# Optimization experiments

Hardware: AMD Instinct MI355X
Metric: run time of the kernel (lower is better)

## Reference

```python
import jax, jax.numpy as jnp
import numpy as np

B, T, H, V, L = 256, 64, 1024, 128, 32  # batch, enc len, hidden, vocab, max decode len


def setup_inputs() -> dict:
    key = jax.random.key(0)
    ks = jax.random.split(key, 12)
    s = 1.0 / np.sqrt(H)
    inp = {
        "inputs": jax.random.randint(ks[0], (B, T), 0, V, dtype=jnp.int32),
        "max_len": L,
        # encoder params
        "enc_emb": jax.random.normal(ks[1], (V, H), jnp.float32) * 0.02,
        "enc_W": jax.random.normal(ks[2], (H, 4 * H), jnp.float32) * s,
        "enc_U": jax.random.normal(ks[3], (H, 4 * H), jnp.float32) * s,
        "enc_b": jnp.zeros((4 * H,), jnp.float32),
        # decoder params
        "dec_emb": jax.random.normal(ks[4], (V, H), jnp.float32) * 0.02,
        "dec_W": jax.random.normal(ks[5], (H, 4 * H), jnp.float32) * s,
        "dec_U": jax.random.normal(ks[6], (H, 4 * H), jnp.float32) * s,
        "dec_b": jnp.zeros((4 * H,), jnp.float32),
        # output projection
        "out_W": jax.random.normal(ks[7], (H, V), jnp.float32) * s,
        "out_b": jnp.zeros((V,), jnp.float32),
    }
    return inp


def _lstm_step(h, c, x, W, U, b):
    # Keras gate order: input, forget, cell, output
    z = x @ W + h @ U + b  # [B, 4H]
    i, f, g, o = jnp.split(z, 4, axis=-1)
    i = jax.nn.sigmoid(i)
    f = jax.nn.sigmoid(f)
    g = jnp.tanh(g)
    o = jax.nn.sigmoid(o)
    c2 = f * c + i * g
    h2 = o * jnp.tanh(c2)
    return h2, c2


def reference(inputs, max_len, enc_emb, enc_W, enc_U, enc_b,
              dec_emb, dec_W, dec_U, dec_b, out_W, out_b):
    batch = inputs.shape[0]
    hid = enc_W.shape[0]
    vocab = dec_emb.shape[0]
    delimiter = vocab - 1

    # ---- Encoder (mask_zero=True: masked steps carry state through) ----
    x_emb = enc_emb[inputs]                     # [B, T, H]
    mask = (inputs != 0)                        # [B, T]

    def enc_scan(carry, xs):
        h, c = carry
        x_t, m_t = xs                           # [B,H], [B]
        h2, c2 = _lstm_step(h, c, x_t, enc_W, enc_U, enc_b)
        m = m_t[:, None]
        return (jnp.where(m, h2, h), jnp.where(m, c2, c)), None

    h0 = jnp.zeros((batch, hid), x_emb.dtype)
    c0 = jnp.zeros((batch, hid), x_emb.dtype)
    (h, c), _ = jax.lax.scan(enc_scan, (h0, c0),
                             (x_emb.transpose(1, 0, 2), mask.T))

    # ---- Greedy decoder: embed -> LSTM -> dense -> softmax -> argmax ----
    def dec_scan(carry, _):
        h, c, tok = carry
        x = dec_emb[tok]                        # [B, H]
        m = (tok != 0)[:, None]
        h2, c2 = _lstm_step(h, c, x, dec_W, dec_U, dec_b)
        h2 = jnp.where(m, h2, h)
        c2 = jnp.where(m, c2, c)
        y = jax.nn.softmax(h2 @ out_W + out_b)  # [B, V]
        tok2 = jnp.argmax(y, axis=-1).astype(jnp.int32)
        return (h2, c2, tok2), (y, tok2)

    tok0 = jnp.full((batch,), delimiter, jnp.int32)
    _, (ys, toks) = jax.lax.scan(dec_scan, (h, c, tok0), None, length=max_len)
    outputs = ys.transpose(1, 0, 2)             # [B, max_len, V]
    return outputs, toks
```

## Files before the change

### kernel.cpp

```cpp
#include <hip/hip_runtime.h>
#include <hip/hip_bf16.h>

namespace {
constexpr int BATCH = 256;
constexpr int TENC  = 64;
constexpr int HID   = 1024;
constexpr int VOC   = 128;
constexpr int LDEC  = 32;
constexpr int G4    = 4 * HID;
}

using short8 = __attribute__((ext_vector_type(8))) short;
using f32x4  = __attribute__((ext_vector_type(4))) float;

__device__ __forceinline__ void async16(const void* g, void* l) {
  __builtin_amdgcn_global_load_lds(
      (const __attribute__((address_space(1))) void*)g,
      (__attribute__((address_space(3))) void*)l, 16, 0, 0);
}

__device__ __forceinline__ unsigned short f2bf(float x) {
  unsigned int u = __float_as_uint(x);
  return (unsigned short)((u + 0x7fffu + ((u >> 16) & 1u)) >> 16);
}
__device__ __forceinline__ float bf2f(unsigned short h) {
  return __uint_as_float(((unsigned int)h) << 16);
}

__global__ __launch_bounds__(256) void k_init(float* __restrict__ h0,
                                              float* __restrict__ c,
                                              unsigned int* __restrict__ hpk0,
                                              int* __restrict__ tok) {
  int i = blockIdx.x * 256 + threadIdx.x;
  h0[i] = 0.f;
  c[i]  = 0.f;
  hpk0[i] = 0u;
  if (i < BATCH) tok[i] = VOC - 1;
}

__global__ __launch_bounds__(256) void k_split_u(
    const float* __restrict__ enc_U, const float* __restrict__ dec_U,
    unsigned short* __restrict__ enc_hi, unsigned short* __restrict__ enc_lo,
    unsigned short* __restrict__ dec_hi, unsigned short* __restrict__ dec_lo) {
  const float* U;
  unsigned short *hi_p, *lo_p;
  if (blockIdx.y == 0) { U = enc_U; hi_p = enc_hi; lo_p = enc_lo; }
  else                 { U = dec_U; hi_p = dec_hi; lo_p = dec_lo; }
  const int gid = blockIdx.x * 256 + threadIdx.x;
  const int lanep = gid & 63;
  const int kq = lanep >> 4, coln = lanep & 15;
  const int u = gid >> 6;
  const int f = u & 7;
  const int v2 = u >> 3;
  const int ks = v2 & 31, ct = v2 >> 5;
  const int n = (f >> 1) * HID + ct * 32 + (f & 1) * 16 + coln;
  const int kbase = ks * 32 + kq * 8;

  unsigned short hv[8], lv[8];
#pragma unroll
  for (int kk = 0; kk < 8; ++kk) {
    const float x = U[(size_t)(kbase + kk) * G4 + n];
    hv[kk] = f2bf(x);
    lv[kk] = f2bf(x - bf2f(hv[kk]));
  }
  *(short8*)(hi_p + (size_t)gid * 8) = *(short8*)hv;
  *(short8*)(lo_p + (size_t)gid * 8) = *(short8*)lv;
}

__global__ __launch_bounds__(256) void k_precompute(
    const float* __restrict__ enc_emb, const float* __restrict__ enc_W,
    const float* __restrict__ enc_b,   const float* __restrict__ dec_emb,
    const float* __restrict__ dec_W,   const float* __restrict__ dec_b,
    float* __restrict__ P_enc, float* __restrict__ P_dec) {
  const float* emb; const float* W; const float* bias; float* P;
  if (blockIdx.z == 0) { emb = enc_emb; W = enc_W; bias = enc_b; P = P_enc; }
  else                 { emb = dec_emb; W = dec_W; bias = dec_b; P = P_dec; }

  __shared__ float A_s[2][64][32];
  __shared__ float B_s[2][32][64];

  const int t    = threadIdx.x;
  const int col0 = blockIdx.x * 64;
  const int v0   = blockIdx.y * 64;
  const int tx   = t & 15;
  const int ty   = t >> 4;
  const int a_row = t >> 3, a_kq = (t & 7) * 4;
  const int b_k   = t >> 4, b_cq = (t & 15) * 4;

  float acc[4][4];
#pragma unroll
  for (int r = 0; r < 4; ++r)
#pragma unroll
    for (int j = 0; j < 4; ++j) acc[r][j] = 0.f;

  async16(&emb[(v0 + a_row) * HID + a_kq], &A_s[0][a_row][a_kq]);
  async16(&emb[(v0 + 32 + a_row) * HID + a_kq], &A_s[0][32 + a_row][a_kq]);
  async16(&W[b_k * G4 + col0 + b_cq], &B_s[0][b_k][b_cq]);
  async16(&W[(16 + b_k) * G4 + col0 + b_cq], &B_s[0][16 + b_k][b_cq]);

  for (int tile = 0; tile < 32; ++tile) {
    const int buf = tile & 1;
    __syncthreads();
    if (tile < 31) {
      const int nb = buf ^ 1;
      const int k0 = (tile + 1) * 32;
      async16(&emb[(v0 + a_row) * HID + k0 + a_kq], &A_s[nb][a_row][a_kq]);
      async16(&emb[(v0 + 32 + a_row) * HID + k0 + a_kq],
              &A_s[nb][32 + a_row][a_kq]);
      async16(&W[(k0 + b_k) * G4 + col0 + b_cq], &B_s[nb][b_k][b_cq]);
      async16(&W[(k0 + 16 + b_k) * G4 + col0 + b_cq],
              &B_s[nb][16 + b_k][b_cq]);
    }
#pragma unroll
    for (int k4 = 0; k4 < 32; k4 += 4) {
      float4 av[4];
#pragma unroll
      for (int r = 0; r < 4; ++r)
        av[r] = *(const float4*)&A_s[buf][ty * 4 + r][k4];
#pragma unroll
      for (int q = 0; q < 4; ++q) {
        const float4 b = *(const float4*)&B_s[buf][k4 + q][tx * 4];
#pragma unroll
        for (int r = 0; r < 4; ++r) {
          const float a = ((const float*)&av[r])[q];
          acc[r][0] += a * b.x;
          acc[r][1] += a * b.y;
          acc[r][2] += a * b.z;
          acc[r][3] += a * b.w;
        }
      }
    }
  }

  const float4 b4 = *(const float4*)&bias[col0 + tx * 4];
#pragma unroll
  for (int r = 0; r < 4; ++r) {
    float4 o;
    o.x = acc[r][0] + b4.x;
    o.y = acc[r][1] + b4.y;
    o.z = acc[r][2] + b4.z;
    o.w = acc[r][3] + b4.w;
    *(float4*)&P[(v0 + ty * 4 + r) * G4 + col0 + tx * 4] = o;
  }
}

__global__ __launch_bounds__(256, 1) void k_cell(
    const float* __restrict__ h_in, float* __restrict__ h_out,
    float* __restrict__ c,
    const unsigned short* __restrict__ Upk_hi,
    const unsigned short* __restrict__ Upk_lo,
    const unsigned short* __restrict__ hpk_in,
    unsigned short* __restrict__ hpk_out,
    const float* __restrict__ P, const int* __restrict__ tok_idx,
    int tok_stride) {
  const int bx = blockIdx.x;
  const int ct = bx & 31;
  const int rt = bx >> 5;
  const int j0 = ct * 32;
  const int r0 = rt * 32;
  const int t    = threadIdx.x;
  const int lane = t & 63;
  const int g    = t >> 6;

  __shared__ float z_s[32][132];

  const unsigned short* pa[2][2];
  const unsigned short* pb[2][2];
#pragma unroll
  for (int m = 0; m < 2; ++m)
#pragma unroll
    for (int s = 0; s < 2; ++s)
      pa[m][s] = hpk_in + ((((s * 32) * 16 + (rt * 2 + m)) * 64 + lane) << 3);
#pragma unroll
  for (int nf = 0; nf < 2; ++nf) {
    pb[nf][0] = Upk_hi + (((ct * 32 * 8 + (g * 2 + nf)) * 64 + lane) << 3);
    pb[nf][1] = Upk_lo + (((ct * 32 * 8 + (g * 2 + nf)) * 64 + lane) << 3);
  }
  constexpr int ASTR = 16 * 64 * 8;
  constexpr int BSTR = 8 * 64 * 8;

  short8 a[4][2][2], b[4][2][2];
  f32x4 acc[2][2];
#pragma unroll
  for (int m = 0; m < 2; ++m)
#pragma unroll
    for (int n = 0; n < 2; ++n) acc[m][n] = (f32x4){0.f, 0.f, 0.f, 0.f};

#define LOADT(T, p)                                                          \
  {                                                                          \
    _Pragma("unroll") for (int m = 0; m < 2; ++m)                            \
        _Pragma("unroll") for (int s = 0; s < 2; ++s)                        \
            a[p][m][s] = *(const short8*)(pa[m][s] + (T) * ASTR);            \
    _Pragma("unroll") for (int nf = 0; nf < 2; ++nf)                         \
        _Pragma("unroll") for (int s = 0; s < 2; ++s)                        \
            b[p][nf][s] = *(const short8*)(pb[nf][s] + (T) * BSTR);          \
  }
#define MFMAT(p)                                                             \
  _Pragma("unroll") for (int m = 0; m < 2; ++m)                              \
      _Pragma("unroll") for (int n = 0; n < 2; ++n) {                        \
    acc[m][n] = __builtin_amdgcn_mfma_f32_16x16x32_bf16(                     \
        a[p][m][0], b[p][n][0], acc[m][n], 0, 0, 0);                         \
    acc[m][n] = __builtin_amdgcn_mfma_f32_16x16x32_bf16(                     \
        a[p][m][0], b[p][n][1], acc[m][n], 0, 0, 0);                         \
    acc[m][n] = __builtin_amdgcn_mfma_f32_16x16x32_bf16(                     \
        a[p][m][1], b[p][n][0], acc[m][n], 0, 0, 0);                         \
    acc[m][n] = __builtin_amdgcn_mfma_f32_16x16x32_bf16(                     \
        a[p][m][1], b[p][n][1], acc[m][n], 0, 0, 0);                         \
  }

  LOADT(0, 0)
  LOADT(1, 1)
  LOADT(2, 2)
  LOADT(3, 3)

  for (int T = 0; T < 32; T += 4) {
    MFMAT(0)
    if (T + 4 < 32) LOADT(T + 4, 0)
    MFMAT(1)
    if (T + 5 < 32) LOADT(T + 5, 1)
    MFMAT(2)
    if (T + 6 < 32) LOADT(T + 6, 2)
    MFMAT(3)
    if (T + 7 < 32) LOADT(T + 7, 3)
  }
#undef LOADT
#undef MFMAT

#pragma unroll
  for (int m = 0; m < 2; ++m)
#pragma unroll
    for (int n = 0; n < 2; ++n)
#pragma unroll
      for (int r = 0; r < 4; ++r) {
        const int row = m * 16 + (lane >> 4) * 4 + r;
        const int col = n * 16 + (lane & 15);
        z_s[row][g * 32 + col] = acc[m][n][r];
      }
  __syncthreads();

  const int hc = t & 31;
#pragma unroll
  for (int p = 0; p < 4; ++p) {
    const int row  = (t >> 5) * 4 + p;
    const int grow = r0 + row;
    const int token = tok_idx[grow * tok_stride];
    const float* Px = P + (size_t)token * G4;
    const int col = j0 + hc;
    const float zi = z_s[row][hc]      + Px[col];
    const float zf = z_s[row][32 + hc] + Px[HID + col];
    const float zg = z_s[row][64 + hc] + Px[2 * HID + col];
    const float zo = z_s[row][96 + hc] + Px[3 * HID + col];
    const float ig = 1.f / (1.f + expf(-zi));
    const float fg = 1.f / (1.f + expf(-zf));
    const float gg = tanhf(zg);
    const float og = 1.f / (1.f + expf(-zo));
    const float c_old = c[grow * HID + col];
    const float c2 = fg * c_old + ig * gg;
    const float h2 = og * tanhf(c2);
    float hfin;
    if (token != 0) {
      hfin = h2;
      h_out[grow * HID + col] = h2;
      c[grow * HID + col]     = c2;
    } else {
      hfin = h_in[grow * HID + col];
      h_out[grow * HID + col] = hfin;
    }
    const unsigned short hi = f2bf(hfin);
    const unsigned short lo = f2bf(hfin - bf2f(hi));
    const int kq = hc >> 3, kk = hc & 7;
    const int base =
        ((((ct) * 16 + (grow >> 4)) * 64 + kq * 16 + (grow & 15)) << 3) + kk;
    hpk_out[base] = hi;
    hpk_out[(32 * 16 * 64 << 3) + base] = lo;
  }
}

__global__ __launch_bounds__(128) void k_logits(
    const float* __restrict__ h, const float* __restrict__ out_W,
    const float* __restrict__ out_b, float* __restrict__ out, int t,
    int* __restrict__ tok) {
  const int b0 = blockIdx.x * 2;
  const int v  = threadIdx.x;

  __shared__ float h_s[2][HID];
  __shared__ float red_v[128];
  __shared__ int   red_i[128];

#pragma unroll
  for (int i = 0; i < 4; ++i) {
    int q  = v + i * 128;
    int r  = q >> 8;
    int kq = (q & 255) * 4;
    *(float4*)&h_s[r][kq] = *(const float4*)&h[(b0 + r) * HID + kq];
  }
  __syncthreads();

  float acc[2];
  acc[0] = out_b[v];
  acc[1] = acc[0];
#pragma unroll 8
  for (int k = 0; k < HID; ++k) {
    const float w = out_W[k * VOC + v];
    acc[0] += h_s[0][k] * w;
    acc[1] += h_s[1][k] * w;
  }

  for (int r = 0; r < 2; ++r) {
    const int b = b0 + r;
    red_v[v] = acc[r];
    red_i[v] = v;
    __syncthreads();
    for (int s = 64; s > 0; s >>= 1) {
      if (v < s) {
        const float ov = red_v[v + s];
        const int   oi = red_i[v + s];
        if (ov > red_v[v] || (ov == red_v[v] && oi < red_i[v])) {
          red_v[v] = ov;
          red_i[v] = oi;
        }
      }
      __syncthreads();
    }
    const float mx  = red_v[0];
    const int amax  = red_i[0];
    __syncthreads();
    const float e = expf(acc[r] - mx);
    red_v[v] = e;
    __syncthreads();
    for (int s = 64; s > 0; s >>= 1) {
      if (v < s) red_v[v] += red_v[v + s];
      __syncthreads();
    }
    const float sum = red_v[0];
    out[b * (LDEC * VOC) + t * VOC + v] = e / sum;
    if (v == 0) {
      tok[b] = amax;
      out[BATCH * LDEC * VOC + t * BATCH + b] = (float)amax;
    }
    __syncthreads();
  }
}

extern "C" void kernel_launch(void* const* d_in, const int* in_sizes, int n_in,
                              void* d_out, int out_size, void* d_ws,
                              size_t ws_size, hipStream_t stream) {
  (void)in_sizes; (void)n_in; (void)out_size; (void)ws_size;
  const int*   inputs  = (const int*)d_in[0];
  const float* enc_emb = (const float*)d_in[2];
  const float* enc_W   = (const float*)d_in[3];
  const float* enc_U   = (const float*)d_in[4];
  const float* enc_b   = (const float*)d_in[5];
  const float* dec_emb = (const float*)d_in[6];
  const float* dec_W   = (const float*)d_in[7];
  const float* dec_U   = (const float*)d_in[8];
  const float* dec_b   = (const float*)d_in[9];
  const float* out_W   = (const float*)d_in[10];
  const float* out_b   = (const float*)d_in[11];
  float* out = (float*)d_out;

  float* ws    = (float*)d_ws;
  float* P_enc = ws;
  float* P_dec = P_enc + VOC * G4;
  float* h0    = P_dec + VOC * G4;
  float* h1    = h0 + BATCH * HID;
  float* c     = h1 + BATCH * HID;
  int*   tok   = (int*)(c + BATCH * HID);
  unsigned short* enc_hi = (unsigned short*)(tok + 256);
  unsigned short* enc_lo = enc_hi + (size_t)HID * G4;
  unsigned short* dec_hi = enc_lo + (size_t)HID * G4;
  unsigned short* dec_lo = dec_hi + (size_t)HID * G4;
  unsigned short* hpk0   = dec_lo + (size_t)HID * G4;
  unsigned short* hpk1   = hpk0 + 2 * BATCH * HID;

  k_init<<<(BATCH * HID) / 256, 256, 0, stream>>>(h0, c, (unsigned int*)hpk0,
                                                  tok);

  dim3 sgrid((HID * G4) / 8 / 256, 2);
  k_split_u<<<sgrid, 256, 0, stream>>>(enc_U, dec_U, enc_hi, enc_lo, dec_hi,
                                       dec_lo);

  dim3 pgrid(G4 / 64, 2, 2);
  k_precompute<<<pgrid, 256, 0, stream>>>(enc_emb, enc_W, enc_b, dec_emb,
                                          dec_W, dec_b, P_enc, P_dec);

  float* hin = h0;  float* hout = h1;
  unsigned short* pin = hpk0;  unsigned short* pout = hpk1;
  for (int t = 0; t < TENC; ++t) {
    k_cell<<<256, 256, 0, stream>>>(hin, hout, c, enc_hi, enc_lo, pin, pout,
                                    P_enc, inputs + t, TENC);
    float* tf = hin; hin = hout; hout = tf;
    unsigned short* tp = pin; pin = pout; pout = tp;
  }
  for (int s = 0; s < LDEC; ++s) {
    k_cell<<<256, 256, 0, stream>>>(hin, hout, c, dec_hi, dec_lo, pin, pout,
                                    P_dec, tok, 1);
    k_logits<<<BATCH / 2, 128, 0, stream>>>(hout, out_W, out_b, out, s, tok);
    float* tf = hin; hin = hout; hout = tf;
    unsigned short* tp = pin; pin = pout; pout = tp;
  }
}
```

Measured before the change: 3.121 ms.

## Fuse all encoder/decoder steps into one persistent cooperative kernel with grid sync

Replaces the 64 encoder and 32 pairs of decoder cell/logits launches with a single cooperative kernel that loops over all steps and uses grid.sync between phases. The logits/softmax/argmax stage is folded in, with one block per batch row and the K dimension split across two halves of the block. This is meant to remove per-launch overhead and kernel-boundary gaps on a latency-bound recurrent chain. It also applies an XOR swizzle to the A tile in the precompute GEMM to reduce LDS bank conflicts. The costs are grid-wide barriers, which are not free, and a requirement that all 256 blocks be co-resident.

```diff
diff --git a/kernel.cpp b/kernel.cpp
--- a/kernel.cpp
+++ b/kernel.cpp
@@ -1,5 +1,8 @@
 #include <hip/hip_runtime.h>
 #include <hip/hip_bf16.h>
+#include <hip/hip_cooperative_groups.h>
+
+namespace cg = cooperative_groups;
 
 namespace {
 constexpr int BATCH = 256;
@@ -10,6 +13,7 @@
 constexpr int G4    = 4 * HID;
 }
 
+using ushortt = unsigned short;
 using short8 = __attribute__((ext_vector_type(8))) short;
 using f32x4  = __attribute__((ext_vector_type(4))) float;
 
@@ -19,11 +23,11 @@
       (__attribute__((address_space(3))) void*)l, 16, 0, 0);
 }
 
-__device__ __forceinline__ unsigned short f2bf(float x) {
+__device__ __forceinline__ ushortt f2bf(float x) {
   unsigned int u = __float_as_uint(x);
-  return (unsigned short)((u + 0x7fffu + ((u >> 16) & 1u)) >> 16);
-}
-__device__ __forceinline__ float bf2f(unsigned short h) {
+  return (ushortt)((u + 0x7fffu + ((u >> 16) & 1u)) >> 16);
+}
+__device__ __forceinline__ float bf2f(ushortt h) {
   return __uint_as_float(((unsigned int)h) << 16);
 }
 
@@ -40,10 +44,10 @@
 
 __global__ __launch_bounds__(256) void k_split_u(
     const float* __restrict__ enc_U, const float* __restrict__ dec_U,
-    unsigned short* __restrict__ enc_hi, unsigned short* __restrict__ enc_lo,
-    unsigned short* __restrict__ dec_hi, unsigned short* __restrict__ dec_lo) {
+    ushortt* __restrict__ enc_hi, ushortt* __restrict__ enc_lo,
+    ushortt* __restrict__ dec_hi, ushortt* __restrict__ dec_lo) {
   const float* U;
-  unsigned short *hi_p, *lo_p;
+  ushortt *hi_p, *lo_p;
   if (blockIdx.y == 0) { U = enc_U; hi_p = enc_hi; lo_p = enc_lo; }
   else                 { U = dec_U; hi_p = dec_hi; lo_p = dec_lo; }
   const int gid = blockIdx.x * 256 + threadIdx.x;
@@ -56,7 +60,7 @@
   const int n = (f >> 1) * HID + ct * 32 + (f & 1) * 16 + coln;
   const int kbase = ks * 32 + kq * 8;
 
-  unsigned short hv[8], lv[8];
+  ushortt hv[8], lv[8];
 #pragma unroll
   for (int kk = 0; kk < 8; ++kk) {
     const float x = U[(size_t)(kbase + kk) * G4 + n];
@@ -85,6 +89,7 @@
   const int tx   = t & 15;
   const int ty   = t >> 4;
   const int a_row = t >> 3, a_kq = (t & 7) * 4;
+  const int a_kqs = a_kq ^ ((a_row & 7) << 2);
   const int b_k   = t >> 4, b_cq = (t & 15) * 4;
 
   float acc[4][4];
@@ -93,8 +98,8 @@
 #pragma unroll
     for (int j = 0; j < 4; ++j) acc[r][j] = 0.f;
 
-  async16(&emb[(v0 + a_row) * HID + a_kq], &A_s[0][a_row][a_kq]);
-  async16(&emb[(v0 + 32 + a_row) * HID + a_kq], &A_s[0][32 + a_row][a_kq]);
+  async16(&emb[(v0 + a_row) * HID + a_kqs], &A_s[0][a_row][a_kq]);
+  async16(&emb[(v0 + 32 + a_row) * HID + a_kqs], &A_s[0][32 + a_row][a_kq]);
   async16(&W[b_k * G4 + col0 + b_cq], &B_s[0][b_k][b_cq]);
   async16(&W[(16 + b_k) * G4 + col0 + b_cq], &B_s[0][16 + b_k][b_cq]);
 
@@ -104,8 +109,8 @@
     if (tile < 31) {
       const int nb = buf ^ 1;
       const int k0 = (tile + 1) * 32;
-      async16(&emb[(v0 + a_row) * HID + k0 + a_kq], &A_s[nb][a_row][a_kq]);
-      async16(&emb[(v0 + 32 + a_row) * HID + k0 + a_kq],
+      async16(&emb[(v0 + a_row) * HID + k0 + a_kqs], &A_s[nb][a_row][a_kq]);
+      async16(&emb[(v0 + 32 + a_row) * HID + k0 + a_kqs],
               &A_s[nb][32 + a_row][a_kq]);
       async16(&W[(k0 + b_k) * G4 + col0 + b_cq], &B_s[nb][b_k][b_cq]);
       async16(&W[(k0 + 16 + b_k) * G4 + col0 + b_cq],
@@ -115,8 +120,10 @@
     for (int k4 = 0; k4 < 32; k4 += 4) {
       float4 av[4];
 #pragma unroll
-      for (int r = 0; r < 4; ++r)
-        av[r] = *(const float4*)&A_s[buf][ty * 4 + r][k4];
+      for (int r = 0; r < 4; ++r) {
+        const int rr = ty * 4 + r;
+        av[r] = *(const float4*)&A_s[buf][rr][k4 ^ ((rr & 7) << 2)];
+      }
 #pragma unroll
       for (int q = 0; q < 4; ++q) {
         const float4 b = *(const float4*)&B_s[buf][k4 + q][tx * 4];
@@ -144,15 +151,16 @@
   }
 }
 
-__global__ __launch_bounds__(256, 1) void k_cell(
-    const float* __restrict__ h_in, float* __restrict__ h_out,
-    float* __restrict__ c,
-    const unsigned short* __restrict__ Upk_hi,
-    const unsigned short* __restrict__ Upk_lo,
-    const unsigned short* __restrict__ hpk_in,
-    unsigned short* __restrict__ hpk_out,
-    const float* __restrict__ P, const int* __restrict__ tok_idx,
-    int tok_stride) {
+__global__ __launch_bounds__(256, 1) void k_seq(
+    const int* __restrict__ inputs,
+    const ushortt* __restrict__ enc_hi, const ushortt* __restrict__ enc_lo,
+    const ushortt* __restrict__ dec_hi, const ushortt* __restrict__ dec_lo,
+    const float* __restrict__ P_enc, const float* __restrict__ P_dec,
+    const float* __restrict__ out_W, const float* __restrict__ out_b,
+    float* __restrict__ h0b, float* __restrict__ h1b, float* __restrict__ c,
+    ushortt* __restrict__ hpk0, ushortt* __restrict__ hpk1,
+    int* __restrict__ tok, float* __restrict__ out) {
+  cg::grid_group grid = cg::this_grid();
   const int bx = blockIdx.x;
   const int ct = bx & 31;
   const int rt = bx >> 5;
@@ -163,28 +171,48 @@
   const int g    = t >> 6;
 
   __shared__ float z_s[32][132];
-
-  const unsigned short* pa[2][2];
-  const unsigned short* pb[2][2];
-#pragma unroll
-  for (int m = 0; m < 2; ++m)
-#pragma unroll
-    for (int s = 0; s < 2; ++s)
-      pa[m][s] = hpk_in + ((((s * 32) * 16 + (rt * 2 + m)) * 64 + lane) << 3);
-#pragma unroll
-  for (int nf = 0; nf < 2; ++nf) {
-    pb[nf][0] = Upk_hi + (((ct * 32 * 8 + (g * 2 + nf)) * 64 + lane) << 3);
-    pb[nf][1] = Upk_lo + (((ct * 32 * 8 + (g * 2 + nf)) * 64 + lane) << 3);
-  }
+  __shared__ float h_row[HID];
+  __shared__ float part[VOC];
+  __shared__ float red_v[VOC];
+  __shared__ int   red_i[VOC];
+
   constexpr int ASTR = 16 * 64 * 8;
   constexpr int BSTR = 8 * 64 * 8;
 
-  short8 a[4][2][2], b[4][2][2];
-  f32x4 acc[2][2];
-#pragma unroll
-  for (int m = 0; m < 2; ++m)
-#pragma unroll
-    for (int n = 0; n < 2; ++n) acc[m][n] = (f32x4){0.f, 0.f, 0.f, 0.f};
+#pragma unroll 1
+  for (int step = 0; step < TENC + LDEC; ++step) {
+    const bool enc = step < TENC;
+    const ushortt* Uhi = enc ? enc_hi : dec_hi;
+    const ushortt* Ulo = enc ? enc_lo : dec_lo;
+    const float*   Pp  = enc ? P_enc : P_dec;
+    const int par = step & 1;
+    const ushortt* pin  = par ? hpk1 : hpk0;
+    ushortt*       pout = par ? hpk0 : hpk1;
+    const float*   hin  = par ? h1b : h0b;
+    float*         hout = par ? h0b : h1b;
+    const int* tidx = enc ? (inputs + step) : tok;
+    const int  tstr = enc ? TENC : 1;
+
+    const ushortt* pa[2][2];
+    const ushortt* pb[2][2];
+#pragma unroll
+    for (int m = 0; m < 2; ++m)
+#pragma unroll
+      for (int s = 0; s < 2; ++s)
+        pa[m][s] =
+            pin + ((((s * 32) * 16 + (rt * 2 + m)) * 64 + lane) << 3);
+#pragma unroll
+    for (int nf = 0; nf < 2; ++nf) {
+      pb[nf][0] = Uhi + (((ct * 256 + (g * 2 + nf)) * 64 + lane) << 3);
+      pb[nf][1] = Ulo + (((ct * 256 + (g * 2 + nf)) * 64 + lane) << 3);
+    }
+
+    short8 a[4][2][2], b[4][2][2];
+    f32x4 acc[2][2];
+#pragma unroll
+    for (int m = 0; m < 2; ++m)
+#pragma unroll
+      for (int n = 0; n < 2; ++n) acc[m][n] = (f32x4){0.f, 0.f, 0.f, 0.f};
 
 #define LOADT(T, p)                                                          \
   {                                                                          \
@@ -204,141 +232,126 @@
         a[p][m][0], b[p][n][1], acc[m][n], 0, 0, 0);                         \
     acc[m][n] = __builtin_amdgcn_mfma_f32_16x16x32_bf16(                     \
         a[p][m][1], b[p][n][0], acc[m][n], 0, 0, 0);                         \
-    acc[m][n] = __builtin_amdgcn_mfma_f32_16x16x32_bf16(                     \
-        a[p][m][1], b[p][n][1], acc[m][n], 0, 0, 0);                         \
-  }
-
-  LOADT(0, 0)
-  LOADT(1, 1)
-  LOADT(2, 2)
-  LOADT(3, 3)
-
-  for (int T = 0; T < 32; T += 4) {
-    MFMAT(0)
-    if (T + 4 < 32) LOADT(T + 4, 0)
-    MFMAT(1)
-    if (T + 5 < 32) LOADT(T + 5, 1)
-    MFMAT(2)
-    if (T + 6 < 32) LOADT(T + 6, 2)
-    MFMAT(3)
-    if (T + 7 < 32) LOADT(T + 7, 3)
-  }
+  }
+
+    LOADT(0, 0)
+    LOADT(1, 1)
+    LOADT(2, 2)
+    LOADT(3, 3)
+
+    for (int T = 0; T < 32; T += 4) {
+      MFMAT(0)
+      if (T + 4 < 32) LOADT(T + 4, 0)
+      MFMAT(1)
+      if (T + 5 < 32) LOADT(T + 5, 1)
+      MFMAT(2)
+      if (T + 6 < 32) LOADT(T + 6, 2)
+      MFMAT(3)
+      if (T + 7 < 32) LOADT(T + 7, 3)
+    }
 #undef LOADT
 #undef MFMAT
 
 #pragma unroll
-  for (int m = 0; m < 2; ++m)
-#pragma unroll
-    for (int n = 0; n < 2; ++n)
-#pragma unroll
-      for (int r = 0; r < 4; ++r) {
-        const int row = m * 16 + (lane >> 4) * 4 + r;
-        const int col = n * 16 + (lane & 15);
-        z_s[row][g * 32 + col] = acc[m][n][r];
-      }
-  __syncthreads();
-
-  const int hc = t & 31;
-#pragma unroll
-  for (int p = 0; p < 4; ++p) {
-    const int row  = (t >> 5) * 4 + p;
-    const int grow = r0 + row;
-    const int token = tok_idx[grow * tok_stride];
-    const float* Px = P + (size_t)token * G4;
-    const int col = j0 + hc;
-    const float zi = z_s[row][hc]      + Px[col];
-    const float zf = z_s[row][32 + hc] + Px[HID + col];
-    const float zg = z_s[row][64 + hc] + Px[2 * HID + col];
-    const float zo = z_s[row][96 + hc] + Px[3 * HID + col];
-    const float ig = 1.f / (1.f + expf(-zi));
-    const float fg = 1.f / (1.f + expf(-zf));
-    const float gg = tanhf(zg);
-    const float og = 1.f / (1.f + expf(-zo));
-    const float c_old = c[grow * HID + col];
-    const float c2 = fg * c_old + ig * gg;
-    const float h2 = og * tanhf(c2);
-    float hfin;
-    if (token != 0) {
-      hfin = h2;
-      h_out[grow * HID + col] = h2;
-      c[grow * HID + col]     = c2;
-    } else {
-      hfin = h_in[grow * HID + col];
-      h_out[grow * HID + col] = hfin;
-    }
-    const unsigned short hi = f2bf(hfin);
-    const unsigned short lo = f2bf(hfin - bf2f(hi));
-    const int kq = hc >> 3, kk = hc & 7;
-    const int base =
-        ((((ct) * 16 + (grow >> 4)) * 64 + kq * 16 + (grow & 15)) << 3) + kk;
-    hpk_out[base] = hi;
-    hpk_out[(32 * 16 * 64 << 3) + base] = lo;
-  }
-}
-
-__global__ __launch_bounds__(128) void k_logits(
-    const float* __restrict__ h, const float* __restrict__ out_W,
-    const float* __restrict__ out_b, float* __restrict__ out, int t,
-    int* __restrict__ tok) {
-  const int b0 = blockIdx.x * 2;
-  const int v  = threadIdx.x;
-
-  __shared__ float h_s[2][HID];
-  __shared__ float red_v[128];
-  __shared__ int   red_i[128];
-
-#pragma unroll
-  for (int i = 0; i < 4; ++i) {
-    int q  = v + i * 128;
-    int r  = q >> 8;
-    int kq = (q & 255) * 4;
-    *(float4*)&h_s[r][kq] = *(const float4*)&h[(b0 + r) * HID + kq];
-  }
-  __syncthreads();
-
-  float acc[2];
-  acc[0] = out_b[v];
-  acc[1] = acc[0];
+    for (int m = 0; m < 2; ++m)
+#pragma unroll
+      for (int n = 0; n < 2; ++n)
+#pragma unroll
+        for (int r = 0; r < 4; ++r) {
+          const int row = m * 16 + (lane >> 4) * 4 + r;
+          const int col = n * 16 + (lane & 15);
+          z_s[row][g * 32 + col] = acc[m][n][r];
+        }
+    __syncthreads();
+
+    const int hc = t & 31;
+#pragma unroll
+    for (int p = 0; p < 4; ++p) {
+      const int row  = (t >> 5) * 4 + p;
+      const int grow = r0 + row;
+      const int token = tidx[grow * tstr];
+      const float* Px = Pp + (size_t)token * G4;
+      const int col = j0 + hc;
+      const float zi = z_s[row][hc]      + Px[col];
+      const float zf = z_s[row][32 + hc] + Px[HID + col];
+      const float zg = z_s[row][64 + hc] + Px[2 * HID + col];
+      const float zo = z_s[row][96 + hc] + Px[3 * HID + col];
+      const float ig = 1.f / (1.f + expf(-zi));
+      const float fg = 1.f / (1.f + expf(-zf));
+      const float gg = tanhf(zg);
+      const float og = 1.f / (1.f + expf(-zo));
+      const float c_old = c[grow * HID + col];
+      const float c2 = fg * c_old + ig * gg;
+      const float h2 = og * tanhf(c2);
+      float hfin;
+      if (token != 0) {
+        hfin = h2;
+        hout[grow * HID + col] = h2;
+        c[grow * HID + col]    = c2;
+      } else {
+        hfin = hin[grow * HID + col];
+        hout[grow * HID + col] = hfin;
+      }
+      const ushortt hi = f2bf(hfin);
+      const ushortt lo = f2bf(hfin - bf2f(hi));
+      const int kq = hc >> 3, kk = hc & 7;
+      const int base =
+          ((((ct)*16 + (grow >> 4)) * 64 + kq * 16 + (grow & 15)) << 3) + kk;
+      pout[base] = hi;
+      pout[(32 * 16 * 64 << 3) + base] = lo;
+    }
+    __syncthreads();
+    grid.sync();
+
+    if (!enc) {
+      const int drow = bx;
+      *(float4*)&h_row[t * 4] = *(const float4*)&hout[drow * HID + t * 4];
+      __syncthreads();
+      const int v = t & 127, kh = t >> 7;
+      float accl = (kh == 0) ? out_b[v] : 0.f;
+      const float* wp = out_W + (size_t)(kh * 512) * VOC + v;
+      const float* hp = h_row + kh * 512;
 #pragma unroll 8
-  for (int k = 0; k < HID; ++k) {
-    const float w = out_W[k * VOC + v];
-    acc[0] += h_s[0][k] * w;
-    acc[1] += h_s[1][k] * w;
-  }
-
-  for (int r = 0; r < 2; ++r) {
-    const int b = b0 + r;
-    red_v[v] = acc[r];
-    red_i[v] = v;
-    __syncthreads();
-    for (int s = 64; s > 0; s >>= 1) {
-      if (v < s) {
-        const float ov = red_v[v + s];
-        const int   oi = red_i[v + s];
-        if (ov > red_v[v] || (ov == red_v[v] && oi < red_i[v])) {
-          red_v[v] = ov;
-          red_i[v] = oi;
+      for (int k = 0; k < 512; ++k) accl += hp[k] * wp[(size_t)k * VOC];
+      if (kh) part[v] = accl;
+      __syncthreads();
+      const float full = accl + ((kh == 0) ? part[v] : 0.f);
+      if (kh == 0) { red_v[v] = full; red_i[v] = v; }
+      __syncthreads();
+      for (int s = 64; s > 0; s >>= 1) {
+        if (t < s) {
+          const float ov = red_v[t + s];
+          const int   oi = red_i[t + s];
+          if (ov > red_v[t] || (ov == red_v[t] && oi < red_i[t])) {
+            red_v[t] = ov;
+            red_i[t] = oi;
+          }
         }
-      }
-      __syncthreads();
-    }
-    const float mx  = red_v[0];
-    const int amax  = red_i[0];
-    __syncthreads();
-    const float e = expf(acc[r] - mx);
-    red_v[v] = e;
-    __syncthreads();
-    for (int s = 64; s > 0; s >>= 1) {
-      if (v < s) red_v[v] += red_v[v + s];
-      __syncthreads();
-    }
-    const float sum = red_v[0];
-    out[b * (LDEC * VOC) + t * VOC + v] = e / sum;
-    if (v == 0) {
-      tok[b] = amax;
-      out[BATCH * LDEC * VOC + t * BATCH + b] = (float)amax;
-    }
-    __syncthreads();
+        __syncthreads();
+      }
+      const float mx = red_v[0];
+      const int amax = red_i[0];
+      __syncthreads();
+      float e = 0.f;
+      if (kh == 0) {
+        e = expf(full - mx);
+        red_v[v] = e;
+      }
+      __syncthreads();
+      for (int s = 64; s > 0; s >>= 1) {
+        if (t < s) red_v[t] += red_v[t + s];
+        __syncthreads();
+      }
+      const int ds = step - TENC;
+      if (kh == 0)
+        out[(size_t)drow * (LDEC * VOC) + ds * VOC + v] = e / red_v[0];
+      if (t == 0) {
+        tok[drow] = amax;
+        out[(size_t)BATCH * LDEC * VOC + ds * BATCH + drow] = (float)amax;
+      }
+      __syncthreads();
+      grid.sync();
+    }
   }
 }
 
@@ -366,12 +379,12 @@
   float* h1    = h0 + BATCH * HID;
   float* c     = h1 + BATCH * HID;
   int*   tok   = (int*)(c + BATCH * HID);
-  unsigned short* enc_hi = (unsigned short*)(tok + 256);
-  unsigned short* enc_lo = enc_hi + (size_t)HID * G4;
-  unsigned short* dec_hi = enc_lo + (size_t)HID * G4;
-  unsigned short* dec_lo = dec_hi + (size_t)HID * G4;
-  unsigned short* hpk0   = dec_lo + (size_t)HID * G4;
-  unsigned short* hpk1   = hpk0 + 2 * BATCH * HID;
+  ushortt* enc_hi = (ushortt*)(tok + 256);
+  ushortt* enc_lo = enc_hi + (size_t)HID * G4;
+  ushortt* dec_hi = enc_lo + (size_t)HID * G4;
+  ushortt* dec_lo = dec_hi + (size_t)HID * G4;
+  ushortt* hpk0   = dec_lo + (size_t)HID * G4;
+  ushortt* hpk1   = hpk0 + 2 * BATCH * HID;
 
   k_init<<<(BATCH * HID) / 256, 256, 0, stream>>>(h0, c, (unsigned int*)hpk0,
                                                   tok);
@@ -384,19 +397,12 @@
   k_precompute<<<pgrid, 256, 0, stream>>>(enc_emb, enc_W, enc_b, dec_emb,
                                           dec_W, dec_b, P_enc, P_dec);
 
-  float* hin = h0;  float* hout = h1;
-  unsigned short* pin = hpk0;  unsigned short* pout = hpk1;
-  for (int t = 0; t < TENC; ++t) {
-    k_cell<<<256, 256, 0, stream>>>(hin, hout, c, enc_hi, enc_lo, pin, pout,
-                                    P_enc, inputs + t, TENC);
-    float* tf = hin; hin = hout; hout = tf;
-    unsigned short* tp = pin; pin = pout; pout = tp;
-  }
-  for (int s = 0; s < LDEC; ++s) {
-    k_cell<<<256, 256, 0, stream>>>(hin, hout, c, dec_hi, dec_lo, pin, pout,
-                                    P_dec, tok, 1);
-    k_logits<<<BATCH / 2, 128, 0, stream>>>(hout, out_W, out_b, out, s, tok);
-    float* tf = hin; hin = hout; hout = tf;
-    unsigned short* tp = pin; pin = pout; pout = tp;
-  }
-}
+  void* kargs[] = {(void*)&inputs, (void*)&enc_hi, (void*)&enc_lo,
+                   (void*)&dec_hi, (void*)&dec_lo, (void*)&P_enc,
+                   (void*)&P_dec,  (void*)&out_W,  (void*)&out_b,
+                   (void*)&h0,     (void*)&h1,     (void*)&c,
+                   (void*)&hpk0,   (void*)&hpk1,   (void*)&tok,
+                   (void*)&out};
+  hipLaunchCooperativeKernel((void*)k_seq, dim3(256), dim3(256), kargs, 0,
+                             stream);
+}
```

Result: slower. 6.996 ms (+124.2%).
